# Optimization experiments

Hardware: AMD Instinct MI355X
Metric: run time of the kernel (lower is better)

The kernel has to match this reference:

```python
import jax, jax.numpy as jnp
import numpy as np

FEATURE_DIM = 256
HEADS = 8


def setup_inputs() -> dict:
    key = jax.random.key(0)
    ks = jax.random.split(key, 9)
    d, h = FEATURE_DIM, HEADS
    b, n = 4, 4096
    s_in = 1.0 / np.sqrt(d)
    s_out = 1.0 / np.sqrt(d * h)
    return {
        "x": jax.random.normal(ks[0], (b, n, d), dtype=jnp.float32),
        "Wq": jax.random.uniform(ks[1], (d, d * h), jnp.float32, -s_in, s_in),
        "bq": jax.random.uniform(ks[2], (d * h,), jnp.float32, -s_in, s_in),
        "Wk": jax.random.uniform(ks[3], (d, d * h), jnp.float32, -s_in, s_in),
        "bk": jax.random.uniform(ks[4], (d * h,), jnp.float32, -s_in, s_in),
        "Wv": jax.random.uniform(ks[5], (d, d * h), jnp.float32, -s_in, s_in),
        "bv": jax.random.uniform(ks[6], (d * h,), jnp.float32, -s_in, s_in),
        "Wo": jax.random.uniform(ks[7], (d * h, d), jnp.float32, -s_out, s_out),
        "bo": jax.random.uniform(ks[8], (d,), jnp.float32, -s_out, s_out),
    }


def reference(x, Wq, bq, Wk, bk, Wv, bv, Wo, bo):
    b, n, d = x.shape
    h = HEADS
    scale = d ** (-0.5)
    # projections: (b, n, h, d) -- note: NO head transpose, matching original
    q = (x @ Wq + bq).reshape(b, n, h, d)
    k = (x @ Wk + bk).reshape(b, n, h, d)
    v = (x @ Wv + bv).reshape(b, n, h, d)
    # attention is head-vs-head per token: (b, n, h, h)
    attn = jnp.einsum("bnhd,bngd->bnhg", q, k) * scale
    attn = jax.nn.softmax(attn, axis=-1)
    out = jnp.einsum("bnhg,bngd->bnhd", attn, v).reshape(b, n, h * d)
    return out @ Wo + bo
```

## Files before the change

kernel.cpp:

```cpp
#include <hip/hip_runtime.h>
#include <hip/hip_bf16.h>
#include <math.h>

typedef __bf16 bf16;
typedef __bf16 bf16x4 __attribute__((ext_vector_type(4)));
typedef __bf16 bf16x8 __attribute__((ext_vector_type(8)));
typedef float f32x4 __attribute__((ext_vector_type(4)));
typedef unsigned int u32;
typedef u32 __attribute__((address_space(1))) gu32;
typedef u32 __attribute__((address_space(3))) lu32;

#define TOK   16384
#define D_    256
#define HD    2048
#define VN    2048

#define GLDS16(g, l) __builtin_amdgcn_global_load_lds((gu32*)(g), (lu32*)(l), 16, 0, 0)
#define WAIT_VM(n)  __builtin_amdgcn_s_waitcnt(0x0F70 | (n))
#define WAIT_LGKM0  __builtin_amdgcn_s_waitcnt(0xC07F)
#define BAR() do { __builtin_amdgcn_s_barrier(); __builtin_amdgcn_sched_barrier(0); } while (0)

__device__ __forceinline__ void transpose_body(
    const void* __restrict__ src, bf16* __restrict__ dst, int R, int C,
    int tc, int tr, int f, int mode, float (*tile)[33])
{
    int lx = threadIdx.x & 31, ly = threadIdx.x >> 5;
    for (int i = 0; i < 4; i++) {
        int r = ly + i * 8;
        size_t idx = (size_t)(tr + r) * C + tc + lx;
        tile[r][lx] = f ? ((const float*)src)[idx] : (float)((const bf16*)src)[idx];
    }
    __syncthreads();
    for (int i = 0; i < 4; i++) {
        int r = ly + i * 8;
        int k = tr + lx;
        int n = tc + r;
        size_t di;
        if (mode == 1)
            di = (size_t)n * 2048 + ((k & 255) << 3) + (k >> 8);
        else if (mode == 2)
            di = (size_t)(4096 + ((n & 255) << 3) + (n >> 8)) * 256 + k;
        else if (mode == 3)
            di = (size_t)((((n & 255) >> 4) << 8) + ((n >> 8) << 4) + (n & 15)) * 256 + k;
        else if (mode == 4)
            di = (size_t)((((n & 255) >> 4) << 8) + 128 + ((n >> 8) << 4) + (n & 15)) * 256 + k;
        else
            di = (size_t)n * R + k;
        dst[di] = (bf16)tile[lx][r];
    }
}

__global__ __launch_bounds__(256) void prep(
    const void* __restrict__ x,
    const void* __restrict__ Wq, const void* __restrict__ bq,
    const void* __restrict__ Wk, const void* __restrict__ bk,
    const void* __restrict__ Wv, const void* __restrict__ bv,
    const void* __restrict__ Wo, const void* __restrict__ bo,
    bf16* __restrict__ xb, bf16* __restrict__ WTI, bf16* __restrict__ WoT,
    bf16* __restrict__ bqkv, bf16* __restrict__ bob)
{
    __shared__ float tile[32][33];
    __shared__ int sflag;
    int tid = threadIdx.x;
    if (tid == 0) sflag = 0;
    __syncthreads();
    {
        float v = fabsf((float)((const bf16*)x)[2 * tid]);
        if (!(v < 1e4f)) sflag = 1;
    }
    __syncthreads();
    int f = sflag;
    int b = blockIdx.x;

    if (b < 4096) {
        int i = b * 256 + tid;
        bf16x4 o;
        if (f) { f32x4 v = ((const f32x4*)x)[i]; for (int e = 0; e < 4; e++) o[e] = (bf16)v[e]; }
        else   { o = ((const bf16x4*)x)[i]; }
        ((bf16x4*)xb)[i] = o;
    } else if (b < 4121) {
        int i = (b - 4096) * 256 + tid;
        if (i < 6400) {
            const void* src; bf16* dst = bqkv; int off, woff;
            if (i < 2048) {
                src = bq; off = i;
                int d = off & 255, h = off >> 8;
                woff = ((d >> 4) << 8) + (h << 4) + (d & 15);
            } else if (i < 4096) {
                src = bk; off = i - 2048;
                int d = off & 255, h = off >> 8;
                woff = ((d >> 4) << 8) + 128 + (h << 4) + (d & 15);
            } else if (i < 6144) {
                src = bv; off = i - 4096;
                woff = 4096 + ((off & 255) << 3) + (off >> 8);
            } else {
                src = bo; dst = bob; off = i - 6144; woff = off;
            }
            float v = f ? ((const float*)src)[off] : (float)((const bf16*)src)[off];
            dst[woff] = (bf16)v;
        }
        __syncthreads();
    } else if (b < 5657) {
        int idx = b - 4121;
        int tx = idx & 63, rest = idx >> 6;
        int ty = rest & 7, tz = rest >> 3;
        const void* src = (tz == 0) ? Wq : (tz == 1) ? Wk : Wv;
        int mode = (tz == 0) ? 3 : (tz == 1) ? 4 : 2;
        transpose_body(src, WTI, 256, 2048, tx * 32, ty * 32, f, mode, tile);
    } else {
        int idx = b - 5657;
        int tx = idx & 7, ty = idx >> 3;
        transpose_body(Wo, WoT, 2048, 256, tx * 32, ty * 32, f, 1, tile);
    }
}

__global__ __launch_bounds__(512, 2) void qkv_score(
    const bf16* __restrict__ X, const bf16* __restrict__ WTI,
    const bf16* __restrict__ bI, bf16* __restrict__ vout, float* __restrict__ P)
{
    __shared__ bf16 Ws[2][64 * 256];
    __shared__ bf16 qkh[64 * 256];
    int tid = threadIdx.x, wave = tid >> 6, lane = tid & 63;
    int mrow = lane & 15, quad = lane >> 4;
    int wm3 = (wave >> 2) * 32, wn3 = (wave & 3) * 16;
    int h = lane >> 3, g = lane & 7;
    int t0 = blockIdx.x * 64;

#pragma unroll
    for (int i = 0; i < 4; i++) {
        int row = (i * 8 + wave) * 2 + (lane >> 5);
        int sl = lane & 31;
        int gc = (sl & 24) | ((sl & 7) ^ (row & 7));
        GLDS16(&X[(size_t)(t0 + row) * 256 + gc * 8], &Ws[0][(i * 8 + wave) * 512]);
    }
    WAIT_VM(0);
    BAR();
    bf16x8 areg[2][8];
#pragma unroll
    for (int mt = 0; mt < 2; mt++)
#pragma unroll
        for (int ks = 0; ks < 8; ks++) {
            int arow = wm3 + mt * 16 + mrow;
            int sl = ks * 4 + quad;
            int ph = (sl & 24) | ((sl & 7) ^ (arow & 7));
            areg[mt][ks] = *(const bf16x8*)&Ws[0][arow * 256 + ph * 8];
        }
    WAIT_LGKM0;
    BAR();

#pragma unroll
    for (int i = 0; i < 4; i++) {
        int row = (i * 8 + wave) * 2 + (lane >> 5);
        int sl = lane & 31;
        int gc = (sl & 24) | ((sl & 7) ^ (row & 7));
        GLDS16(&WTI[(size_t)row * 256 + gc * 8], &Ws[0][(i * 8 + wave) * 512]);
    }

    float S[8] = {};

    for (int s = 0; s < 96; s++) {
        int cur = s & 1;
        if (s < 95) {
#pragma unroll
            for (int i = 0; i < 4; i++) {
                int row = (i * 8 + wave) * 2 + (lane >> 5);
                int sl = lane & 31;
                int gc = (sl & 24) | ((sl & 7) ^ (row & 7));
                GLDS16(&WTI[(size_t)((s + 1) * 64 + row) * 256 + gc * 8],
                       &Ws[cur ^ 1][(i * 8 + wave) * 512]);
            }
            WAIT_VM(4);
        } else {
            WAIT_VM(0);
        }
        BAR();

        f32x4 acc0 = {}, acc1 = {};
        int brow = wn3 + mrow;
#pragma unroll
        for (int ks = 0; ks < 8; ks++) {
            int sl = ks * 4 + quad;
            int ph = (sl & 24) | ((sl & 7) ^ (brow & 7));
            bf16x8 bv = *(const bf16x8*)&Ws[cur][brow * 256 + ph * 8];
            acc0 = __builtin_amdgcn_mfma_f32_16x16x32_bf16(bv, areg[0][ks], acc0, 0, 0, 0);
            acc1 = __builtin_amdgcn_mfma_f32_16x16x32_bf16(bv, areg[1][ks], acc1, 0, 0, 0);
        }

        if (s < 64) {
            int sub = s & 3, qk = sub >> 1;
            int hh = (sub & 1) * 4 + (wn3 >> 4);
            bf16x4 bb = *(const bf16x4*)&bI[s * 64 + wn3 + quad * 4];
#pragma unroll
            for (int mt = 0; mt < 2; mt++) {
                int t = wm3 + mt * 16 + mrow;
                f32x4 a = mt ? acc1 : acc0;
                bf16x4 o;
#pragma unroll
                for (int r = 0; r < 4; r++) o[r] = (bf16)(a[r] + (float)bb[r]);
                int bo = ((qk << 8) + (hh << 5) + (quad << 3)) ^ ((t & 7) << 4);
                *(bf16x4*)((char*)qkh + t * 512 + bo) = o;
            }
            WAIT_LGKM0;
            BAR();
            if ((s & 3) == 3) {
#pragma unroll
                for (int ti = 0; ti < 8; ti++) {
                    int t = wave * 8 + ti;
                    int swz = (t & 7) << 4;
                    const char* base = (const char*)qkh + t * 512;
                    bf16x8 q0 = *(const bf16x8*)(base + (((h << 5)) ^ swz));
                    bf16x8 q1 = *(const bf16x8*)(base + (((h << 5) + 16) ^ swz));
                    bf16x8 k0 = *(const bf16x8*)(base + ((256 + (g << 5)) ^ swz));
                    bf16x8 k1 = *(const bf16x8*)(base + ((256 + (g << 5) + 16) ^ swz));
                    float a = 0.f;
#pragma unroll
                    for (int e = 0; e < 8; e++)
                        a += (float)q0[e] * (float)k0[e] + (float)q1[e] * (float)k1[e];
                    S[ti] += a;
                }
                WAIT_LGKM0;
            }
        } else {
            int sv = s - 64;
            bf16* ep = qkh;
            bf16x4 bb = *(const bf16x4*)&bI[s * 64 + wn3 + quad * 4];
#pragma unroll
            for (int mt = 0; mt < 2; mt++) {
                int t = wm3 + mt * 16 + mrow;
                f32x4 a = mt ? acc1 : acc0;
                bf16x4 o;
#pragma unroll
                for (int r = 0; r < 4; r++) o[r] = (bf16)(a[r] + (float)bb[r]);
                *(bf16x4*)&ep[t * 72 + wn3 + quad * 4] = o;
            }
            WAIT_LGKM0;
            BAR();
            {
                int tt = tid >> 3, c8 = (tid & 7) * 8;
                bf16x8 val = *(const bf16x8*)&ep[tt * 72 + c8];
                *(bf16x8*)&vout[(size_t)(t0 + tt) * VN + sv * 64 + c8] = val;
            }
            BAR();
        }
    }

#pragma unroll
    for (int ti = 0; ti < 8; ti++) {
        int t = t0 + wave * 8 + ti;
        float sc = S[ti] * 0.0625f;
        float m = sc;
        for (int off = 1; off < 8; off <<= 1) m = fmaxf(m, __shfl_xor(m, off, 8));
        float p = __expf(sc - m);
        float sum = p;
        for (int off = 1; off < 8; off <<= 1) sum += __shfl_xor(sum, off, 8);
        P[(size_t)t * 64 + lane] = p / sum;
    }
}

__global__ __launch_bounds__(256) void out_fused(
    const bf16* __restrict__ vb, const bf16* __restrict__ WoT,
    const float* __restrict__ P, const bf16* __restrict__ bob,
    float* __restrict__ outp)
{
    __shared__ bf16 Bs[2][256 * 64];
    __shared__ bf16 Vs[2][32 * 64];
    int m0 = blockIdx.x * 32;
    int tid = threadIdx.x, wave = tid >> 6, lane = tid & 63;
    int wm = (wave >> 1) * 16, wn = (wave & 1) * 128;
    int mrow = lane & 15, quad = lane >> 4;
    int t = wm + mrow, ts = t & 7;
    int sl8 = lane >> 3, sl = lane & 7;

    float Pv[64];
    {
        const float* pr = P + (size_t)(m0 + t) * 64;
#pragma unroll
        for (int j = 0; j < 16; j++) {
            f32x4 v4 = *(const f32x4*)&pr[j * 4];
            Pv[4 * j + 0] = v4[0]; Pv[4 * j + 1] = v4[1];
            Pv[4 * j + 2] = v4[2]; Pv[4 * j + 3] = v4[3];
        }
    }

    f32x4 acc[8] = {};
    {
        int tt = (wave << 3) + sl8;
        GLDS16(&vb[(size_t)(m0 + tt) * VN + ((sl ^ (tt & 7)) << 3)],
               &Vs[0][wave * 512]);
#pragma unroll
        for (int i = 0; i < 8; i++) {
            int n = (wave << 6) + (i << 3) + sl8;
            GLDS16(&WoT[(size_t)n * HD + ((sl ^ (n & 7)) << 3)],
                   &Bs[0][((wave << 6) + (i << 3)) << 6]);
        }
    }

    for (int c = 0; c < 32; c++) {
        __syncthreads();
        if (c < 31) {
            int cc = c + 1, bb = cc & 1;
            int tt = (wave << 3) + sl8;
            GLDS16(&vb[(size_t)(m0 + tt) * VN + cc * 64 + ((sl ^ (tt & 7)) << 3)],
                   &Vs[bb][wave * 512]);
#pragma unroll
            for (int i = 0; i < 8; i++) {
                int n = (wave << 6) + (i << 3) + sl8;
                GLDS16(&WoT[(size_t)n * HD + cc * 64 + ((sl ^ (n & 7)) << 3)],
                       &Bs[bb][((wave << 6) + (i << 3)) << 6]);
            }
        }
        const bf16* Vb = Vs[c & 1];
        const bf16* Bb = Bs[c & 1];

        bf16x8 vf0 = *(const bf16x8*)&Vb[(t << 6) + ((quad ^ ts) << 3)];
        bf16x8 vf1 = *(const bf16x8*)&Vb[(t << 6) + (((quad + 4) ^ ts) << 3)];
        float v0f[8], v1f[8];
#pragma unroll
        for (int e = 0; e < 8; e++) { v0f[e] = (float)vf0[e]; v1f[e] = (float)vf1[e]; }
        bf16x8 af0, af1;
#pragma unroll
        for (int hh = 0; hh < 8; hh++) {
            float a0 = 0.f, a1 = 0.f;
#pragma unroll
            for (int gg = 0; gg < 8; gg++) {
                a0 += Pv[hh * 8 + gg] * v0f[gg];
                a1 += Pv[hh * 8 + gg] * v1f[gg];
            }
            af0[hh] = (bf16)a0; af1[hh] = (bf16)a1;
        }
#pragma unroll
        for (int nt = 0; nt < 8; nt++) {
            bf16x8 bv = *(const bf16x8*)&Bb[(wn + nt * 16 + mrow) * 64
                            + ((quad ^ (mrow & 7)) << 3)];
            acc[nt] = __builtin_amdgcn_mfma_f32_16x16x32_bf16(bv, af0, acc[nt], 0, 0, 0);
        }
#pragma unroll
        for (int nt = 0; nt < 8; nt++) {
            bf16x8 bv = *(const bf16x8*)&Bb[(wn + nt * 16 + mrow) * 64
                            + (((4 + quad) ^ (mrow & 7)) << 3)];
            acc[nt] = __builtin_amdgcn_mfma_f32_16x16x32_bf16(bv, af1, acc[nt], 0, 0, 0);
        }
    }

    int row = m0 + wm + mrow;
#pragma unroll
    for (int nt = 0; nt < 8; nt++) {
        int col = wn + nt * 16 + quad * 4;
        bf16x4 bb = *(const bf16x4*)&bob[col];
        f32x4 o;
        for (int r = 0; r < 4; r++) o[r] = acc[nt][r] + (float)bb[r];
        *(f32x4*)&outp[(size_t)row * D_ + col] = o;
    }
}

extern "C" void kernel_launch(void* const* d_in, const int* in_sizes, int n_in,
                              void* d_out, int out_size, void* d_ws, size_t ws_size,
                              hipStream_t stream)
{
    const void* x  = d_in[0];
    const void* Wq = d_in[1];
    const void* bq = d_in[2];
    const void* Wk = d_in[3];
    const void* bk = d_in[4];
    const void* Wv = d_in[5];
    const void* bv = d_in[6];
    const void* Wo = d_in[7];
    const void* bo = d_in[8];
    float* out = (float*)d_out;

    char* ws = (char*)d_ws;
    bf16*  vbuf = (bf16*)ws;
    bf16*  WTI  = (bf16*)(ws + 67108864);
    bf16*  WoT  = (bf16*)(ws + 70254592);
    bf16*  xb   = (bf16*)(ws + 71303168);
    bf16*  bqkv = (bf16*)(ws + 79691776);
    bf16*  bob  = (bf16*)(ws + 79704064);
    float* Pbuf = (float*)(ws + 79704576);

    prep<<<6169, 256, 0, stream>>>(x, Wq, bq, Wk, bk, Wv, bv, Wo, bo,
                                   xb, WTI, WoT, bqkv, bob);
    qkv_score<<<256, 512, 0, stream>>>(xb, WTI, bqkv, vbuf, Pbuf);
    out_fused<<<512, 256, 0, stream>>>(vbuf, WoT, Pbuf, bob, out);
}
```

Measured before the change: 271.8 us.

## Split V projection into separate tiled GEMM kernel and triple-buffer QK score loop

Moves the V projection out of the fused QKV/score kernel into a standalone 128x128-tiled MFMA GEMM launched over many more blocks. The remaining QK score kernel keeps only the 64 Q/K slices, uses a three-deep LDS ring so weight loads run two steps ahead, and drops the per-step barrier except at the score accumulation points. The aim is better parallelism than 256 blocks for the V work and less barrier stall in the score loop. The cost is an extra kernel launch, re-reading X for V, and more shared memory per block, which may limit occupancy.

```diff
diff --git a/kernel.cpp b/kernel.cpp
--- a/kernel.cpp
+++ b/kernel.cpp
@@ -114,11 +114,69 @@
     }
 }
 
-__global__ __launch_bounds__(512, 2) void qkv_score(
+__global__ __launch_bounds__(256) void v_proj(
+    const bf16* __restrict__ X, const bf16* __restrict__ WT,
+    const bf16* __restrict__ bI, bf16* __restrict__ vout)
+{
+    __shared__ char smem[36864];
+    bf16* As = (bf16*)smem;
+    bf16* Bs = (bf16*)(smem + 16384);
+    int m0 = blockIdx.y * 128, n0 = blockIdx.x * 128;
+    int tid = threadIdx.x, wave = tid >> 6, lane = tid & 63;
+    int wm = (wave >> 1) * 64, wn = (wave & 1) * 64;
+    int mrow = lane & 15, quad = lane >> 4;
+    int lrow8 = lane >> 3, lslot = lane & 7;
+
+    f32x4 acc[4][4] = {};
+    for (int k0 = 0; k0 < D_; k0 += 64) {
+        __syncthreads();
+        for (int i = 0; i < 4; i++) {
+            int rbase = wave * 32 + i * 8;
+            int row = rbase + lrow8;
+            int gc = lslot ^ (row & 7);
+            GLDS16(&X[(size_t)(m0 + row) * D_ + k0 + gc * 8], &As[rbase * 64]);
+            GLDS16(&WT[(size_t)(n0 + row) * D_ + k0 + gc * 8], &Bs[rbase * 64]);
+        }
+        __syncthreads();
+        for (int kk = 0; kk < 64; kk += 32) {
+            int slot = (((kk >> 3) + quad) ^ (mrow & 7)) * 8;
+            bf16x8 af[4], bfv[4];
+            for (int mt = 0; mt < 4; mt++)
+                af[mt] = *(const bf16x8*)&As[(wm + mt * 16 + mrow) * 64 + slot];
+            for (int nt = 0; nt < 4; nt++)
+                bfv[nt] = *(const bf16x8*)&Bs[(wn + nt * 16 + mrow) * 64 + slot];
+            for (int mt = 0; mt < 4; mt++)
+                for (int nt = 0; nt < 4; nt++)
+                    acc[mt][nt] = __builtin_amdgcn_mfma_f32_16x16x32_bf16(
+                        bfv[nt], af[mt], acc[mt][nt], 0, 0, 0);
+        }
+    }
+
+    __syncthreads();
+    bf16* ep = (bf16*)smem + wave * (64 * 72);
+    for (int mt = 0; mt < 4; mt++) {
+        for (int nt = 0; nt < 4; nt++) {
+            int col = n0 + wn + nt * 16 + quad * 4;
+            bf16x4 bb = *(const bf16x4*)&bI[col];
+            bf16x4 o;
+            for (int r = 0; r < 4; r++) o[r] = (bf16)(acc[mt][nt][r] + (float)bb[r]);
+            *(bf16x4*)&ep[(mt * 16 + mrow) * 72 + nt * 16 + quad * 4] = o;
+        }
+    }
+    __syncthreads();
+    for (int i = 0; i < 8; i++) {
+        int r = i * 8 + (lane >> 3);
+        int cb = (lane & 7) * 8;
+        bf16x8 val = *(const bf16x8*)&ep[r * 72 + cb];
+        *(bf16x8*)&vout[(size_t)(m0 + wm + r) * VN + n0 + wn + cb] = val;
+    }
+}
+
+__global__ __launch_bounds__(512, 2) void qk_score(
     const bf16* __restrict__ X, const bf16* __restrict__ WTI,
-    const bf16* __restrict__ bI, bf16* __restrict__ vout, float* __restrict__ P)
-{
-    __shared__ bf16 Ws[2][64 * 256];
+    const bf16* __restrict__ bI, float* __restrict__ P)
+{
+    __shared__ bf16 Ws[3][64 * 256];
     __shared__ bf16 qkh[64 * 256];
     int tid = threadIdx.x, wave = tid >> 6, lane = tid & 63;
     int mrow = lane & 15, quad = lane >> 4;
@@ -131,23 +189,10 @@
         int row = (i * 8 + wave) * 2 + (lane >> 5);
         int sl = lane & 31;
         int gc = (sl & 24) | ((sl & 7) ^ (row & 7));
-        GLDS16(&X[(size_t)(t0 + row) * 256 + gc * 8], &Ws[0][(i * 8 + wave) * 512]);
+        GLDS16(&X[(size_t)(t0 + row) * 256 + gc * 8], &Ws[2][(i * 8 + wave) * 512]);
     }
     WAIT_VM(0);
     BAR();
-    bf16x8 areg[2][8];
-#pragma unroll
-    for (int mt = 0; mt < 2; mt++)
-#pragma unroll
-        for (int ks = 0; ks < 8; ks++) {
-            int arow = wm3 + mt * 16 + mrow;
-            int sl = ks * 4 + quad;
-            int ph = (sl & 24) | ((sl & 7) ^ (arow & 7));
-            areg[mt][ks] = *(const bf16x8*)&Ws[0][arow * 256 + ph * 8];
-        }
-    WAIT_LGKM0;
-    BAR();
-
 #pragma unroll
     for (int i = 0; i < 4; i++) {
         int row = (i * 8 + wave) * 2 + (lane >> 5);
@@ -155,92 +200,92 @@
         int gc = (sl & 24) | ((sl & 7) ^ (row & 7));
         GLDS16(&WTI[(size_t)row * 256 + gc * 8], &Ws[0][(i * 8 + wave) * 512]);
     }
+#pragma unroll
+    for (int i = 0; i < 4; i++) {
+        int row = (i * 8 + wave) * 2 + (lane >> 5);
+        int sl = lane & 31;
+        int gc = (sl & 24) | ((sl & 7) ^ (row & 7));
+        GLDS16(&WTI[(size_t)(64 + row) * 256 + gc * 8], &Ws[1][(i * 8 + wave) * 512]);
+    }
+    bf16x8 areg[2][8];
+#pragma unroll
+    for (int mt = 0; mt < 2; mt++)
+#pragma unroll
+        for (int ks = 0; ks < 8; ks++) {
+            int arow = wm3 + mt * 16 + mrow;
+            int sl = ks * 4 + quad;
+            int ph = (sl & 24) | ((sl & 7) ^ (arow & 7));
+            areg[mt][ks] = *(const bf16x8*)&Ws[2][arow * 256 + ph * 8];
+        }
+    WAIT_LGKM0;
+    BAR();
 
     float S[8] = {};
 
-    for (int s = 0; s < 96; s++) {
-        int cur = s & 1;
-        if (s < 95) {
+    for (int s = 0; s < 64; s++) {
+        int cur = s % 3;
+        if (s == 63) { WAIT_VM(0); } else { WAIT_VM(4); }
+        BAR();
+        if (s <= 61) {
+            int nb = (s + 2) % 3;
 #pragma unroll
             for (int i = 0; i < 4; i++) {
                 int row = (i * 8 + wave) * 2 + (lane >> 5);
                 int sl = lane & 31;
                 int gc = (sl & 24) | ((sl & 7) ^ (row & 7));
-                GLDS16(&WTI[(size_t)((s + 1) * 64 + row) * 256 + gc * 8],
-                       &Ws[cur ^ 1][(i * 8 + wave) * 512]);
+                GLDS16(&WTI[(size_t)((s + 2) * 64 + row) * 256 + gc * 8],
+                       &Ws[nb][(i * 8 + wave) * 512]);
             }
-            WAIT_VM(4);
-        } else {
-            WAIT_VM(0);
-        }
-        BAR();
-
-        f32x4 acc0 = {}, acc1 = {};
+        }
+
         int brow = wn3 + mrow;
+        bf16x8 bv[8];
 #pragma unroll
         for (int ks = 0; ks < 8; ks++) {
             int sl = ks * 4 + quad;
             int ph = (sl & 24) | ((sl & 7) ^ (brow & 7));
-            bf16x8 bv = *(const bf16x8*)&Ws[cur][brow * 256 + ph * 8];
-            acc0 = __builtin_amdgcn_mfma_f32_16x16x32_bf16(bv, areg[0][ks], acc0, 0, 0, 0);
-            acc1 = __builtin_amdgcn_mfma_f32_16x16x32_bf16(bv, areg[1][ks], acc1, 0, 0, 0);
-        }
-
-        if (s < 64) {
-            int sub = s & 3, qk = sub >> 1;
-            int hh = (sub & 1) * 4 + (wn3 >> 4);
-            bf16x4 bb = *(const bf16x4*)&bI[s * 64 + wn3 + quad * 4];
-#pragma unroll
-            for (int mt = 0; mt < 2; mt++) {
-                int t = wm3 + mt * 16 + mrow;
-                f32x4 a = mt ? acc1 : acc0;
-                bf16x4 o;
-#pragma unroll
-                for (int r = 0; r < 4; r++) o[r] = (bf16)(a[r] + (float)bb[r]);
-                int bo = ((qk << 8) + (hh << 5) + (quad << 3)) ^ ((t & 7) << 4);
-                *(bf16x4*)((char*)qkh + t * 512 + bo) = o;
+            bv[ks] = *(const bf16x8*)&Ws[cur][brow * 256 + ph * 8];
+        }
+        f32x4 acc0 = {}, acc1 = {};
+#pragma unroll
+        for (int ks = 0; ks < 8; ks++) {
+            acc0 = __builtin_amdgcn_mfma_f32_16x16x32_bf16(bv[ks], areg[0][ks], acc0, 0, 0, 0);
+            acc1 = __builtin_amdgcn_mfma_f32_16x16x32_bf16(bv[ks], areg[1][ks], acc1, 0, 0, 0);
+        }
+
+        int sub = s & 3, qk = sub >> 1;
+        int hh = (sub & 1) * 4 + (wn3 >> 4);
+        bf16x4 bb = *(const bf16x4*)&bI[s * 64 + wn3 + quad * 4];
+#pragma unroll
+        for (int mt = 0; mt < 2; mt++) {
+            int t = wm3 + mt * 16 + mrow;
+            f32x4 a = mt ? acc1 : acc0;
+            bf16x4 o;
+#pragma unroll
+            for (int r = 0; r < 4; r++) o[r] = (bf16)(a[r] + (float)bb[r]);
+            int bo = ((qk << 8) + (hh << 5) + (quad << 3)) ^ ((t & 7) << 4);
+            *(bf16x4*)((char*)qkh + t * 512 + bo) = o;
+        }
+
+        if ((s & 3) == 3) {
+            WAIT_LGKM0;
+            BAR();
+#pragma unroll
+            for (int ti = 0; ti < 8; ti++) {
+                int t = wave * 8 + ti;
+                int swz = (t & 7) << 4;
+                const char* base = (const char*)qkh + t * 512;
+                bf16x8 q0 = *(const bf16x8*)(base + (((h << 5)) ^ swz));
+                bf16x8 q1 = *(const bf16x8*)(base + (((h << 5) + 16) ^ swz));
+                bf16x8 k0 = *(const bf16x8*)(base + ((256 + (g << 5)) ^ swz));
+                bf16x8 k1 = *(const bf16x8*)(base + ((256 + (g << 5) + 16) ^ swz));
+                float a = 0.f;
+#pragma unroll
+                for (int e = 0; e < 8; e++)
+                    a += (float)q0[e] * (float)k0[e] + (float)q1[e] * (float)k1[e];
+                S[ti] += a;
             }
             WAIT_LGKM0;
-            BAR();
-            if ((s & 3) == 3) {
-#pragma unroll
-                for (int ti = 0; ti < 8; ti++) {
-                    int t = wave * 8 + ti;
-                    int swz = (t & 7) << 4;
-                    const char* base = (const char*)qkh + t * 512;
-                    bf16x8 q0 = *(const bf16x8*)(base + (((h << 5)) ^ swz));
-                    bf16x8 q1 = *(const bf16x8*)(base + (((h << 5) + 16) ^ swz));
-                    bf16x8 k0 = *(const bf16x8*)(base + ((256 + (g << 5)) ^ swz));
-                    bf16x8 k1 = *(const bf16x8*)(base + ((256 + (g << 5) + 16) ^ swz));
-                    float a = 0.f;
-#pragma unroll
-                    for (int e = 0; e < 8; e++)
-                        a += (float)q0[e] * (float)k0[e] + (float)q1[e] * (float)k1[e];
-                    S[ti] += a;
-                }
-                WAIT_LGKM0;
-            }
-        } else {
-            int sv = s - 64;
-            bf16* ep = qkh;
-            bf16x4 bb = *(const bf16x4*)&bI[s * 64 + wn3 + quad * 4];
-#pragma unroll
-            for (int mt = 0; mt < 2; mt++) {
-                int t = wm3 + mt * 16 + mrow;
-                f32x4 a = mt ? acc1 : acc0;
-                bf16x4 o;
-#pragma unroll
-                for (int r = 0; r < 4; r++) o[r] = (bf16)(a[r] + (float)bb[r]);
-                *(bf16x4*)&ep[t * 72 + wn3 + quad * 4] = o;
-            }
-            WAIT_LGKM0;
-            BAR();
-            {
-                int tt = tid >> 3, c8 = (tid & 7) * 8;
-                bf16x8 val = *(const bf16x8*)&ep[tt * 72 + c8];
-                *(bf16x8*)&vout[(size_t)(t0 + tt) * VN + sv * 64 + c8] = val;
-            }
-            BAR();
         }
     }
 
@@ -379,6 +424,7 @@
 
     prep<<<6169, 256, 0, stream>>>(x, Wq, bq, Wk, bk, Wv, bv, Wo, bo,
                                    xb, WTI, WoT, bqkv, bob);
-    qkv_score<<<256, 512, 0, stream>>>(xb, WTI, bqkv, vbuf, Pbuf);
+    qk_score<<<256, 512, 0, stream>>>(xb, WTI, bqkv, Pbuf);
+    v_proj<<<dim3(16, 128), 256, 0, stream>>>(xb, WTI + 4096 * 256, bqkv + 4096, vbuf);
     out_fused<<<512, 256, 0, stream>>>(vbuf, WoT, Pbuf, bob, out);
 }
```

Result: no change. 270.3 us (-0.5%).
